# Optimization experiments

Measured on AMD Instinct MI355X. Metric: run time of the kernel, lower is better.

Reference implementation:

```python
import jax, jax.numpy as jnp
import numpy as np

OUT_F, IN_F, RANK, GROUP = 8192, 8192, 16, 128
N_GROUPS = OUT_F * IN_F // GROUP  # 524288
TOKENS = 256


def block_dequantize_2bit(weight_q2, weight_norm):
    """weight_q2: [n_groups, GROUP//4] int (uint8 values), weight_norm: [n_groups, 1] fp16.
    Each byte packs 4 two-bit codes little-endian (code k in bits 2k..2k+1).
    Code q in {0..3} dequantizes to ((q/3)*2 - 1) * norm."""
    shifts = jnp.array([0, 2, 4, 6], dtype=jnp.int32)
    q = (weight_q2[:, :, None] >> shifts) & 3          # [n_groups, GROUP//4, 4]
    q = q.reshape(weight_q2.shape[0], -1).astype(jnp.float32)  # [n_groups, GROUP]
    return (q * (2.0 / 3.0) - 1.0) * weight_norm.astype(jnp.float32)


def setup_inputs() -> dict:
    key = jax.random.key(0)
    ks = jax.random.split(key, 6)
    x = jax.random.normal(ks[0], (TOKENS, IN_F), dtype=jnp.float32)
    weight_q2 = jax.random.randint(ks[1], (N_GROUPS, GROUP // 4), 0, 256, dtype=jnp.int32)
    weight_norm = jax.random.uniform(ks[2], (N_GROUPS, 1), dtype=jnp.float16, minval=0.01, maxval=1.0)
    bias = jax.random.normal(ks[3], (OUT_F,), dtype=jnp.float32)
    lora_a = jax.random.normal(ks[4], (RANK, IN_F), dtype=jnp.float32) * 0.02
    lora_b = jax.random.normal(ks[5], (OUT_F, RANK), dtype=jnp.float32) * 0.02
    return {"x": x, "weight_q2": weight_q2, "weight_norm": weight_norm,
            "bias": bias, "lora_a": lora_a, "lora_b": lora_b}


def reference(x, weight_q2, weight_norm, bias, lora_a, lora_b):
    x_f32 = x.astype(jnp.float32)
    W = block_dequantize_2bit(weight_q2, weight_norm).reshape(OUT_F, IN_F)  # fp32 [out, in]
    base_out = x_f32 @ W.T + bias                       # [tokens, out]
    lora_out = (x_f32 @ lora_a.T) @ lora_b.T            # [tokens, out]
    return (base_out + lora_out).astype(x.dtype)
```

## Files before the change

kernel.cpp:

```cpp
#include <hip/hip_runtime.h>
#include <hip/hip_fp16.h>

typedef unsigned int u32;
typedef unsigned short u16;
typedef int i32x4 __attribute__((ext_vector_type(4)));
typedef float f32x4 __attribute__((ext_vector_type(4)));

#define OUT_F 8192
#define IN_F 8192
#define TOKENS 256
#define N_GROUPS 524288
#define SPLITK 4
#define KSPAN (IN_F / SPLITK)
#define KT (KSPAN / 64)

#define XQ_OFF 0
#define T_OFF ((size_t)TOKENS * IN_F)
#define SX_OFF (T_OFF + 32768)
#define NF_OFF (SX_OFF + 2048)
#define PART_OFF (NF_OFF + (size_t)N_GROUPS * 2)
#define PART_BYTES ((size_t)SPLITK * TOKENS * OUT_F * 4)
#define WS_NEED (PART_OFF + PART_BYTES)

__device__ __forceinline__ u32 unpack4(u32 b) {
  u32 e = ((b & 0x33u) * 0x2002u) & 0x00060006u;
  u32 o = ((b & 0xCCu) * 0x80080u) & 0x06000600u;
  return ((e | o) + 0x7D7D7D7Du) ^ 0x80808080u;
}

__global__ __launch_bounds__(256) void prep(const void* __restrict__ wn,
                                            __half* __restrict__ nf,
                                            const float* __restrict__ x,
                                            const float* __restrict__ la,
                                            signed char* __restrict__ xq,
                                            float* __restrict__ sx,
                                            float* __restrict__ t) {
  int tid = threadIdx.x;
  if (blockIdx.x < 512) {
    __shared__ int votes[3];
    __shared__ u16 tile[64][17];
    if (tid < 3) votes[tid] = 0;
    __syncthreads();
    const u16* pu = (const u16*)wn;
    const u32* pw = (const u32*)wn;
    int v16 = 0, vbf = 0, vf = 0;
    for (int i = tid; i < 2048; i += 256) {
      u16 u = pu[i];
      float h = __half2float(__builtin_bit_cast(__half, u));
      float b = __builtin_bit_cast(float, ((u32)u) << 16);
      if (h > 0.008f && h < 1.002f) v16++;
      if (b > 0.008f && b < 1.002f) vbf++;
    }
    for (int i = tid; i < 1024; i += 256) {
      float f = __builtin_bit_cast(float, pw[i]);
      if (f > 0.008f && f < 1.002f) vf++;
    }
    atomicAdd(&votes[0], v16);
    atomicAdd(&votes[1], vbf);
    atomicAdd(&votes[2], vf);
    __syncthreads();
    int a16 = votes[0], abf = votes[1], af32 = 2 * votes[2];
    int mode = (a16 >= abf && a16 >= af32) ? 0 : (abf >= af32 ? 1 : 2);
    int nb = blockIdx.x * 16;
#pragma unroll
    for (int i = 0; i < 4; ++i) {
      int idx = i * 256 + tid;
      int g = idx & 63, nl = idx >> 6;
      int flat = (nb + nl) * 64 + g;
      float v;
      if (mode == 0) v = __half2float(((const __half*)wn)[flat]);
      else if (mode == 1) v = __builtin_bit_cast(float, ((u32)((const u16*)wn)[flat]) << 16);
      else v = ((const float*)wn)[flat];
      tile[g][nl] = __builtin_bit_cast(u16, __float2half(v));
    }
    __syncthreads();
#pragma unroll
    for (int i = 0; i < 4; ++i) {
      int idx = i * 256 + tid;
      int go = idx >> 4, no = idx & 15;
      ((u16*)nf)[(size_t)go * 8192 + nb + no] = tile[go][no];
    }
    return;
  }
  int b2 = blockIdx.x - 512;
  int m = b2 & 255;
  int half = b2 >> 8;
  const float4* xr = (const float4*)(x + (size_t)m * IN_F);
  float4 xv[4];
  float am = 0.f;
  float pl[16];
#pragma unroll
  for (int r = 0; r < 16; ++r) pl[r] = 0.f;
#pragma unroll
  for (int it = 0; it < 4; ++it) {
    int k4 = half * 1024 + it * 256 + tid;
    xv[it] = xr[k4];
    am = fmaxf(am, fmaxf(fmaxf(fabsf(xv[it].x), fabsf(xv[it].y)),
                         fmaxf(fabsf(xv[it].z), fabsf(xv[it].w))));
#pragma unroll
    for (int r = 0; r < 16; ++r) {
      const float4 av = ((const float4*)(la + (size_t)r * IN_F))[k4];
      pl[r] = fmaf(xv[it].x, av.x, pl[r]);
      pl[r] = fmaf(xv[it].y, av.y, pl[r]);
      pl[r] = fmaf(xv[it].z, av.z, pl[r]);
      pl[r] = fmaf(xv[it].w, av.w, pl[r]);
    }
  }
#pragma unroll
  for (int d = 32; d > 0; d >>= 1) am = fmaxf(am, __shfl_xor(am, d));
#pragma unroll
  for (int r = 0; r < 16; ++r) {
    float v = pl[r];
#pragma unroll
    for (int d = 32; d > 0; d >>= 1) v += __shfl_xor(v, d);
    pl[r] = v;
  }
  __shared__ float red[4][16];
  __shared__ float amS[4];
  int wave = tid >> 6, lane = tid & 63;
  if (lane == 0) {
    amS[wave] = am;
#pragma unroll
    for (int r = 0; r < 16; ++r) red[wave][r] = pl[r];
  }
  __syncthreads();
  am = fmaxf(fmaxf(amS[0], amS[1]), fmaxf(amS[2], amS[3]));
  float inv = (am > 1e-20f) ? 127.f / am : 0.f;
  u32* xqw = (u32*)(xq + (size_t)m * IN_F);
#pragma unroll
  for (int it = 0; it < 4; ++it) {
    int k4 = half * 1024 + it * 256 + tid;
    int q0 = (int)rintf(xv[it].x * inv);
    int q1 = (int)rintf(xv[it].y * inv);
    int q2 = (int)rintf(xv[it].z * inv);
    int q3 = (int)rintf(xv[it].w * inv);
    xqw[k4] = (q0 & 255) | ((q1 & 255) << 8) | ((q2 & 255) << 16) | ((q3 & 255) << 24);
  }
  if (tid == 0) sx[half * 256 + m] = am / 127.f;
  if (tid < 16)
    t[((size_t)half * TOKENS + m) * 16 + tid] =
        red[0][tid] + red[1][tid] + red[2][tid] + red[3][tid];
}

__global__ __launch_bounds__(256) void prep2(const float* __restrict__ t,
                                             const float* __restrict__ lb,
                                             const float* __restrict__ bias,
                                             float* __restrict__ out) {
  __shared__ float tS[16 * 16];
  int tid = threadIdx.x;
  int n = blockIdx.x * 256 + tid;
  int mbase = blockIdx.y * 16;
  if (tid < 64) {
    float4 a = ((const float4*)(t + (size_t)mbase * 16))[tid];
    float4 b = ((const float4*)(t + (size_t)TOKENS * 16 + (size_t)mbase * 16))[tid];
    ((float4*)tS)[tid] = make_float4(a.x + b.x, a.y + b.y, a.z + b.z, a.w + b.w);
  }
  const float4* lbp = (const float4*)(lb + (size_t)n * 16);
  float4 b0 = lbp[0], b1 = lbp[1], b2 = lbp[2], b3 = lbp[3];
  float bv = bias[n];
  __syncthreads();
#pragma unroll
  for (int mm = 0; mm < 16; ++mm) {
    const float* tr = &tS[mm * 16];
    float a = bv;
    a += tr[0] * b0.x + tr[1] * b0.y + tr[2] * b0.z + tr[3] * b0.w;
    a += tr[4] * b1.x + tr[5] * b1.y + tr[6] * b1.z + tr[7] * b1.w;
    a += tr[8] * b2.x + tr[9] * b2.y + tr[10] * b2.z + tr[11] * b2.w;
    a += tr[12] * b3.x + tr[13] * b3.y + tr[14] * b3.z + tr[15] * b3.w;
    out[(size_t)(mbase + mm) * OUT_F + n] = a;
  }
}

__global__ __launch_bounds__(256) void finish(const float* __restrict__ t,
                                              const float* __restrict__ lb,
                                              const float* __restrict__ bias,
                                              const float* __restrict__ part,
                                              float* __restrict__ out) {
  __shared__ float tS[16 * 16];
  int tid = threadIdx.x;
  int n = blockIdx.x * 256 + tid;
  int mbase = blockIdx.y * 16;
  if (tid < 64) {
    float4 a = ((const float4*)(t + (size_t)mbase * 16))[tid];
    float4 b = ((const float4*)(t + (size_t)TOKENS * 16 + (size_t)mbase * 16))[tid];
    ((float4*)tS)[tid] = make_float4(a.x + b.x, a.y + b.y, a.z + b.z, a.w + b.w);
  }
  const float4* lbp = (const float4*)(lb + (size_t)n * 16);
  float4 b0 = lbp[0], b1 = lbp[1], b2 = lbp[2], b3 = lbp[3];
  float bv = bias[n];
  __syncthreads();
#pragma unroll
  for (int mm = 0; mm < 16; ++mm) {
    const float* tr = &tS[mm * 16];
    float a = bv;
    a += tr[0] * b0.x + tr[1] * b0.y + tr[2] * b0.z + tr[3] * b0.w;
    a += tr[4] * b1.x + tr[5] * b1.y + tr[6] * b1.z + tr[7] * b1.w;
    a += tr[8] * b2.x + tr[9] * b2.y + tr[10] * b2.z + tr[11] * b2.w;
    a += tr[12] * b3.x + tr[13] * b3.y + tr[14] * b3.z + tr[15] * b3.w;
    size_t base = (size_t)(mbase + mm) * OUT_F + n;
#pragma unroll
    for (int kz = 0; kz < SPLITK; ++kz)
      a += part[(size_t)kz * TOKENS * OUT_F + base];
    out[base] = a;
  }
}

__global__ __launch_bounds__(256, 2) void gemm_q2(const signed char* __restrict__ xq,
                                                  const int* __restrict__ wq,
                                                  const __half* __restrict__ nf,
                                                  const float* __restrict__ sx,
                                                  float* __restrict__ dst,
                                                  int mode) {
  __shared__ __align__(16) signed char Bs[2][128 * 64];

  int tid = threadIdx.x;
  int n0 = blockIdx.x * 128;
  int m0 = blockIdx.y * 128;
  int kz = blockIdx.z;
  int kbase = kz * KSPAN;

  int wave = tid >> 6, lane = tid & 63;
  int quad = lane >> 4, l15 = lane & 15;
  int mo = (wave & 1) * 64, no = (wave >> 1) * 64;

  const signed char* gA[4];
#pragma unroll
  for (int mt = 0; mt < 4; ++mt)
    gA[mt] = xq + (size_t)(m0 + mo + mt * 16 + l15) * IN_F + kbase + quad * 16;

  int bn = tid >> 1, h = tid & 1;
  const signed char* gB = (const signed char*)wq + (size_t)(n0 + bn) * IN_F + kbase + h * 32;
  signed char* myB0 = &Bs[0][bn * 64 + h * 32];
  signed char* myB1 = &Bs[1][bn * 64 + h * 32];

  i32x4 zi = {0, 0, 0, 0};
  f32x4 zf = {0.f, 0.f, 0.f, 0.f};
  i32x4 acc[4][4];
  f32x4 accf[4][4];
#pragma unroll
  for (int i = 0; i < 4; ++i)
#pragma unroll
    for (int j = 0; j < 4; ++j) { acc[i][j] = zi; accf[i][j] = zf; }

  i32x4 aF[4], aN[4];
#pragma unroll
  for (int mt = 0; mt < 4; ++mt) aF[mt] = *(const i32x4*)(gA[mt]);
  uint4 w0 = *(const uint4*)(gB);
  uint4 w1 = *(const uint4*)(gB + 16);
  {
    u32 c[8];
    c[0] = unpack4(w0.x); c[1] = unpack4(w0.y); c[2] = unpack4(w0.z); c[3] = unpack4(w0.w);
    c[4] = unpack4(w1.x); c[5] = unpack4(w1.y); c[6] = unpack4(w1.z); c[7] = unpack4(w1.w);
    ((uint4*)myB0)[0] = make_uint4(c[0], c[1], c[2], c[3]);
    ((uint4*)myB0)[1] = make_uint4(c[4], c[5], c[6], c[7]);
  }
  w0 = *(const uint4*)(gB + 64);
  w1 = *(const uint4*)(gB + 80);
  __syncthreads();

#pragma unroll 1
  for (int kt2 = 0; kt2 < KT / 2; ++kt2) {
    int kt = kt2 * 2;

    {
      if (kt + 1 < KT) {
#pragma unroll
        for (int mt = 0; mt < 4; ++mt)
          aN[mt] = *(const i32x4*)(gA[mt] + (kt + 1) * 64);
      }
      {
        u32 c[8];
        c[0] = unpack4(w0.x); c[1] = unpack4(w0.y); c[2] = unpack4(w0.z); c[3] = unpack4(w0.w);
        c[4] = unpack4(w1.x); c[5] = unpack4(w1.y); c[6] = unpack4(w1.z); c[7] = unpack4(w1.w);
        ((uint4*)myB1)[0] = make_uint4(c[0], c[1], c[2], c[3]);
        ((uint4*)myB1)[1] = make_uint4(c[4], c[5], c[6], c[7]);
      }
      if (kt + 2 < KT) {
        w0 = *(const uint4*)(gB + (kt + 2) * 64);
        w1 = *(const uint4*)(gB + (kt + 2) * 64 + 16);
      }
      i32x4 bf[4];
#pragma unroll
      for (int nt = 0; nt < 4; ++nt)
        bf[nt] = *(const i32x4*)(&Bs[0][(no + nt * 16 + l15) * 64 + quad * 16]);
#pragma unroll
      for (int mt = 0; mt < 4; ++mt)
#pragma unroll
        for (int nt = 0; nt < 4; ++nt)
          acc[mt][nt] = __builtin_amdgcn_mfma_i32_16x16x64_i8(aF[mt], bf[nt], acc[mt][nt], 0, 0, 0);
      __syncthreads();
    }

    {
      int ko = kt + 1;
      if (ko + 1 < KT) {
#pragma unroll
        for (int mt = 0; mt < 4; ++mt)
          aF[mt] = *(const i32x4*)(gA[mt] + (ko + 1) * 64);
      }
      int g64 = kz * (KSPAN / 128) + (ko >> 1);
      float nrm[4];
#pragma unroll
      for (int nt = 0; nt < 4; ++nt)
        nrm[nt] = __half2float(nf[(size_t)g64 * 8192 + n0 + no + nt * 16 + l15]) * (1.f / 3.f);
      if (ko + 1 < KT) {
        u32 c[8];
        c[0] = unpack4(w0.x); c[1] = unpack4(w0.y); c[2] = unpack4(w0.z); c[3] = unpack4(w0.w);
        c[4] = unpack4(w1.x); c[5] = unpack4(w1.y); c[6] = unpack4(w1.z); c[7] = unpack4(w1.w);
        ((uint4*)myB0)[0] = make_uint4(c[0], c[1], c[2], c[3]);
        ((uint4*)myB0)[1] = make_uint4(c[4], c[5], c[6], c[7]);
      }
      if (ko + 2 < KT) {
        w0 = *(const uint4*)(gB + (ko + 2) * 64);
        w1 = *(const uint4*)(gB + (ko + 2) * 64 + 16);
      }
      i32x4 bf[4];
#pragma unroll
      for (int nt = 0; nt < 4; ++nt)
        bf[nt] = *(const i32x4*)(&Bs[1][(no + nt * 16 + l15) * 64 + quad * 16]);
#pragma unroll
      for (int mt = 0; mt < 4; ++mt)
#pragma unroll
        for (int nt = 0; nt < 4; ++nt)
          acc[mt][nt] = __builtin_amdgcn_mfma_i32_16x16x64_i8(aN[mt], bf[nt], acc[mt][nt], 0, 0, 0);
#pragma unroll
      for (int nt = 0; nt < 4; ++nt)
#pragma unroll
        for (int mt = 0; mt < 4; ++mt) {
#pragma unroll
          for (int r = 0; r < 4; ++r)
            accf[mt][nt][r] = fmaf((float)acc[mt][nt][r], nrm[nt], accf[mt][nt][r]);
          acc[mt][nt] = zi;
        }
      __syncthreads();
    }
  }

  const float* sxh = sx + (kz >> 1) * 256;
  if (mode) {
    float* pp = dst + (size_t)kz * TOKENS * OUT_F;
#pragma unroll
    for (int mt = 0; mt < 4; ++mt)
#pragma unroll
      for (int r = 0; r < 4; ++r) {
        int mm = m0 + mo + mt * 16 + quad * 4 + r;
        float s = sxh[mm];
#pragma unroll
        for (int nt = 0; nt < 4; ++nt) {
          int nn = n0 + no + nt * 16 + l15;
          pp[(size_t)mm * OUT_F + nn] = accf[mt][nt][r] * s;
        }
      }
  } else {
#pragma unroll
    for (int mt = 0; mt < 4; ++mt)
#pragma unroll
      for (int r = 0; r < 4; ++r) {
        int mm = m0 + mo + mt * 16 + quad * 4 + r;
        float s = sxh[mm];
#pragma unroll
        for (int nt = 0; nt < 4; ++nt) {
          int nn = n0 + no + nt * 16 + l15;
          atomicAdd(&dst[(size_t)mm * OUT_F + nn], accf[mt][nt][r] * s);
        }
      }
  }
}

extern "C" void kernel_launch(void* const* d_in, const int* in_sizes, int n_in,
                              void* d_out, int out_size, void* d_ws, size_t ws_size,
                              hipStream_t stream) {
  (void)in_sizes; (void)n_in; (void)out_size;
  const float* x = (const float*)d_in[0];
  const int* wq = (const int*)d_in[1];
  const void* wn_raw = d_in[2];
  const float* bias = (const float*)d_in[3];
  const float* la = (const float*)d_in[4];
  const float* lb = (const float*)d_in[5];
  float* out = (float*)d_out;

  signed char* xq = (signed char*)((char*)d_ws + XQ_OFF);
  float* t = (float*)((char*)d_ws + T_OFF);
  float* sx = (float*)((char*)d_ws + SX_OFF);
  __half* nf = (__half*)((char*)d_ws + NF_OFF);
  float* part = (float*)((char*)d_ws + PART_OFF);
  int usep = ws_size >= WS_NEED;

  prep<<<1024, 256, 0, stream>>>(wn_raw, nf, x, la, xq, sx, t);
  if (usep) {
    gemm_q2<<<dim3(OUT_F / 128, TOKENS / 128, SPLITK), 256, 0, stream>>>(xq, wq, nf, sx, part, 1);
    finish<<<dim3(OUT_F / 256, TOKENS / 16), 256, 0, stream>>>(t, lb, bias, part, out);
  } else {
    prep2<<<dim3(OUT_F / 256, TOKENS / 16), 256, 0, stream>>>(t, lb, bias, out);
    gemm_q2<<<dim3(OUT_F / 128, TOKENS / 128, SPLITK), 256, 0, stream>>>(xq, wq, nf, sx, out, 0);
  }
}
```

Measured before the change: 172.9 us.

## Load 2-bit weights directly into MFMA registers and split LoRA-A into atomic blocks

The GEMM kernel no longer stages unpacked weights through shared memory with barriers. Each wave loads its own B fragments straight from global memory into registers, unpacks them there, and prefetches the next k-step along with the group norms. Separately, the x·lora_aᵀ product moves out of the quantization blocks into 64 extra blocks that reduce over k-chunks with atomicAdd into a zeroed buffer. This removes LDS traffic and syncthreads from the main loop, at the cost of redundant weight loads across the waves that share an n-tile, an extra memset launch, and nondeterministic float summation order.

New measurement: 216.5 us. 1.25x slower.

```diff
diff --git a/kernel.cpp b/kernel.cpp
--- a/kernel.cpp
+++ b/kernel.cpp
@@ -16,7 +16,7 @@
 
 #define XQ_OFF 0
 #define T_OFF ((size_t)TOKENS * IN_F)
-#define SX_OFF (T_OFF + 32768)
+#define SX_OFF (T_OFF + 16384)
 #define NF_OFF (SX_OFF + 2048)
 #define PART_OFF (NF_OFF + (size_t)N_GROUPS * 2)
 #define PART_BYTES ((size_t)SPLITK * TOKENS * OUT_F * 4)
@@ -82,64 +82,57 @@
     }
     return;
   }
-  int b2 = blockIdx.x - 512;
-  int m = b2 & 255;
-  int half = b2 >> 8;
-  const float4* xr = (const float4*)(x + (size_t)m * IN_F);
-  float4 xv[4];
-  float am = 0.f;
-  float pl[16];
-#pragma unroll
-  for (int r = 0; r < 16; ++r) pl[r] = 0.f;
-#pragma unroll
-  for (int it = 0; it < 4; ++it) {
-    int k4 = half * 1024 + it * 256 + tid;
-    xv[it] = xr[k4];
-    am = fmaxf(am, fmaxf(fmaxf(fabsf(xv[it].x), fabsf(xv[it].y)),
-                         fmaxf(fabsf(xv[it].z), fabsf(xv[it].w))));
+  if (blockIdx.x < 1024) {
+    int b2 = blockIdx.x - 512;
+    int m = b2 & 255;
+    int half = b2 >> 8;
+    const float4* xr = (const float4*)(x + (size_t)m * IN_F);
+    float4 xv[4];
+    float am = 0.f;
+#pragma unroll
+    for (int it = 0; it < 4; ++it) {
+      xv[it] = xr[half * 1024 + it * 256 + tid];
+      am = fmaxf(am, fmaxf(fmaxf(fabsf(xv[it].x), fabsf(xv[it].y)),
+                           fmaxf(fabsf(xv[it].z), fabsf(xv[it].w))));
+    }
+#pragma unroll
+    for (int d = 32; d > 0; d >>= 1) am = fmaxf(am, __shfl_xor(am, d));
+    __shared__ float amS[4];
+    int wave = tid >> 6;
+    if ((tid & 63) == 0) amS[wave] = am;
+    __syncthreads();
+    am = fmaxf(fmaxf(amS[0], amS[1]), fmaxf(amS[2], amS[3]));
+    float inv = (am > 1e-20f) ? 127.f / am : 0.f;
+    u32* xqw = (u32*)(xq + (size_t)m * IN_F);
+#pragma unroll
+    for (int it = 0; it < 4; ++it) {
+      int k4 = half * 1024 + it * 256 + tid;
+      int q0 = (int)rintf(xv[it].x * inv);
+      int q1 = (int)rintf(xv[it].y * inv);
+      int q2 = (int)rintf(xv[it].z * inv);
+      int q3 = (int)rintf(xv[it].w * inv);
+      xqw[k4] = (q0 & 255) | ((q1 & 255) << 8) | ((q2 & 255) << 16) | ((q3 & 255) << 24);
+    }
+    if (tid == 0) sx[half * 256 + m] = am / 127.f;
+    return;
+  }
+  int c = blockIdx.x - 1024;
+  int k0 = c * 128;
+  int m = tid;
+  const float4* xr = (const float4*)(x + (size_t)m * IN_F + k0);
+  float s[16];
+#pragma unroll
+  for (int r = 0; r < 16; ++r) s[r] = 0.f;
+  for (int jj = 0; jj < 32; ++jj) {
+    float4 xv = xr[jj];
 #pragma unroll
     for (int r = 0; r < 16; ++r) {
-      const float4 av = ((const float4*)(la + (size_t)r * IN_F))[k4];
-      pl[r] = fmaf(xv[it].x, av.x, pl[r]);
-      pl[r] = fmaf(xv[it].y, av.y, pl[r]);
-      pl[r] = fmaf(xv[it].z, av.z, pl[r]);
-      pl[r] = fmaf(xv[it].w, av.w, pl[r]);
-    }
-  }
-#pragma unroll
-  for (int d = 32; d > 0; d >>= 1) am = fmaxf(am, __shfl_xor(am, d));
-#pragma unroll
-  for (int r = 0; r < 16; ++r) {
-    float v = pl[r];
-#pragma unroll
-    for (int d = 32; d > 0; d >>= 1) v += __shfl_xor(v, d);
-    pl[r] = v;
-  }
-  __shared__ float red[4][16];
-  __shared__ float amS[4];
-  int wave = tid >> 6, lane = tid & 63;
-  if (lane == 0) {
-    amS[wave] = am;
-#pragma unroll
-    for (int r = 0; r < 16; ++r) red[wave][r] = pl[r];
-  }
-  __syncthreads();
-  am = fmaxf(fmaxf(amS[0], amS[1]), fmaxf(amS[2], amS[3]));
-  float inv = (am > 1e-20f) ? 127.f / am : 0.f;
-  u32* xqw = (u32*)(xq + (size_t)m * IN_F);
-#pragma unroll
-  for (int it = 0; it < 4; ++it) {
-    int k4 = half * 1024 + it * 256 + tid;
-    int q0 = (int)rintf(xv[it].x * inv);
-    int q1 = (int)rintf(xv[it].y * inv);
-    int q2 = (int)rintf(xv[it].z * inv);
-    int q3 = (int)rintf(xv[it].w * inv);
-    xqw[k4] = (q0 & 255) | ((q1 & 255) << 8) | ((q2 & 255) << 16) | ((q3 & 255) << 24);
-  }
-  if (tid == 0) sx[half * 256 + m] = am / 127.f;
-  if (tid < 16)
-    t[((size_t)half * TOKENS + m) * 16 + tid] =
-        red[0][tid] + red[1][tid] + red[2][tid] + red[3][tid];
+      float4 lv = *(const float4*)(la + (size_t)r * IN_F + k0 + jj * 4);
+      s[r] += xv.x * lv.x + xv.y * lv.y + xv.z * lv.z + xv.w * lv.w;
+    }
+  }
+#pragma unroll
+  for (int r = 0; r < 16; ++r) atomicAdd(&t[(size_t)m * 16 + r], s[r]);
 }
 
 __global__ __launch_bounds__(256) void prep2(const float* __restrict__ t,
@@ -150,11 +143,7 @@
   int tid = threadIdx.x;
   int n = blockIdx.x * 256 + tid;
   int mbase = blockIdx.y * 16;
-  if (tid < 64) {
-    float4 a = ((const float4*)(t + (size_t)mbase * 16))[tid];
-    float4 b = ((const float4*)(t + (size_t)TOKENS * 16 + (size_t)mbase * 16))[tid];
-    ((float4*)tS)[tid] = make_float4(a.x + b.x, a.y + b.y, a.z + b.z, a.w + b.w);
-  }
+  if (tid < 64) ((float4*)tS)[tid] = ((const float4*)(t + (size_t)mbase * 16))[tid];
   const float4* lbp = (const float4*)(lb + (size_t)n * 16);
   float4 b0 = lbp[0], b1 = lbp[1], b2 = lbp[2], b3 = lbp[3];
   float bv = bias[n];
@@ -180,11 +169,7 @@
   int tid = threadIdx.x;
   int n = blockIdx.x * 256 + tid;
   int mbase = blockIdx.y * 16;
-  if (tid < 64) {
-    float4 a = ((const float4*)(t + (size_t)mbase * 16))[tid];
-    float4 b = ((const float4*)(t + (size_t)TOKENS * 16 + (size_t)mbase * 16))[tid];
-    ((float4*)tS)[tid] = make_float4(a.x + b.x, a.y + b.y, a.z + b.z, a.w + b.w);
-  }
+  if (tid < 64) ((float4*)tS)[tid] = ((const float4*)(t + (size_t)mbase * 16))[tid];
   const float4* lbp = (const float4*)(lb + (size_t)n * 16);
   float4 b0 = lbp[0], b1 = lbp[1], b2 = lbp[2], b3 = lbp[3];
   float bv = bias[n];
@@ -211,8 +196,6 @@
                                                   const float* __restrict__ sx,
                                                   float* __restrict__ dst,
                                                   int mode) {
-  __shared__ __align__(16) signed char Bs[2][128 * 64];
-
   int tid = threadIdx.x;
   int n0 = blockIdx.x * 128;
   int m0 = blockIdx.y * 128;
@@ -224,14 +207,13 @@
   int mo = (wave & 1) * 64, no = (wave >> 1) * 64;
 
   const signed char* gA[4];
-#pragma unroll
-  for (int mt = 0; mt < 4; ++mt)
-    gA[mt] = xq + (size_t)(m0 + mo + mt * 16 + l15) * IN_F + kbase + quad * 16;
-
-  int bn = tid >> 1, h = tid & 1;
-  const signed char* gB = (const signed char*)wq + (size_t)(n0 + bn) * IN_F + kbase + h * 32;
-  signed char* myB0 = &Bs[0][bn * 64 + h * 32];
-  signed char* myB1 = &Bs[1][bn * 64 + h * 32];
+  const signed char* gB[4];
+#pragma unroll
+  for (int i = 0; i < 4; ++i) {
+    gA[i] = xq + (size_t)(m0 + mo + i * 16 + l15) * IN_F + kbase + quad * 16;
+    gB[i] = (const signed char*)wq + (size_t)(n0 + no + i * 16 + l15) * IN_F + kbase + quad * 16;
+  }
+  const __half* nfg = nf + (size_t)(kz * (KSPAN / 128)) * 8192 + n0 + no + l15;
 
   i32x4 zi = {0, 0, 0, 0};
   f32x4 zf = {0.f, 0.f, 0.f, 0.f};
@@ -242,97 +224,78 @@
 #pragma unroll
     for (int j = 0; j < 4; ++j) { acc[i][j] = zi; accf[i][j] = zf; }
 
-  i32x4 aF[4], aN[4];
-#pragma unroll
-  for (int mt = 0; mt < 4; ++mt) aF[mt] = *(const i32x4*)(gA[mt]);
-  uint4 w0 = *(const uint4*)(gB);
-  uint4 w1 = *(const uint4*)(gB + 16);
-  {
-    u32 c[8];
-    c[0] = unpack4(w0.x); c[1] = unpack4(w0.y); c[2] = unpack4(w0.z); c[3] = unpack4(w0.w);
-    c[4] = unpack4(w1.x); c[5] = unpack4(w1.y); c[6] = unpack4(w1.z); c[7] = unpack4(w1.w);
-    ((uint4*)myB0)[0] = make_uint4(c[0], c[1], c[2], c[3]);
-    ((uint4*)myB0)[1] = make_uint4(c[4], c[5], c[6], c[7]);
-  }
-  w0 = *(const uint4*)(gB + 64);
-  w1 = *(const uint4*)(gB + 80);
-  __syncthreads();
+  uint4 wE[4], wO[4];
+#pragma unroll
+  for (int i = 0; i < 4; ++i) {
+    wE[i] = *(const uint4*)(gB[i]);
+    wO[i] = *(const uint4*)(gB[i] + 64);
+  }
+  float nC[4], nN[4];
+#pragma unroll
+  for (int i = 0; i < 4; ++i) nC[i] = __half2float(nfg[i * 16]) * (1.f / 3.f);
 
 #pragma unroll 1
   for (int kt2 = 0; kt2 < KT / 2; ++kt2) {
     int kt = kt2 * 2;
+    int koE = (kt + 2 < KT ? kt + 2 : KT - 2) * 64;
+    int koO = (kt + 3 < KT ? kt + 3 : KT - 1) * 64;
+    int g2 = (kt2 + 1 < KT / 2 ? kt2 + 1 : kt2);
 
     {
-      if (kt + 1 < KT) {
-#pragma unroll
-        for (int mt = 0; mt < 4; ++mt)
-          aN[mt] = *(const i32x4*)(gA[mt] + (kt + 1) * 64);
-      }
-      {
-        u32 c[8];
-        c[0] = unpack4(w0.x); c[1] = unpack4(w0.y); c[2] = unpack4(w0.z); c[3] = unpack4(w0.w);
-        c[4] = unpack4(w1.x); c[5] = unpack4(w1.y); c[6] = unpack4(w1.z); c[7] = unpack4(w1.w);
-        ((uint4*)myB1)[0] = make_uint4(c[0], c[1], c[2], c[3]);
-        ((uint4*)myB1)[1] = make_uint4(c[4], c[5], c[6], c[7]);
-      }
-      if (kt + 2 < KT) {
-        w0 = *(const uint4*)(gB + (kt + 2) * 64);
-        w1 = *(const uint4*)(gB + (kt + 2) * 64 + 16);
-      }
+      uint4 tW0 = *(const uint4*)(gB[0] + koE);
+      uint4 tW1 = *(const uint4*)(gB[1] + koE);
+      uint4 tW2 = *(const uint4*)(gB[2] + koE);
+      uint4 tW3 = *(const uint4*)(gB[3] + koE);
+      i32x4 aC[4];
+#pragma unroll
+      for (int i = 0; i < 4; ++i) aC[i] = *(const i32x4*)(gA[i] + kt * 64);
+#pragma unroll
+      for (int i = 0; i < 4; ++i)
+        nN[i] = __half2float(nfg[(size_t)g2 * 8192 + i * 16]) * (1.f / 3.f);
       i32x4 bf[4];
 #pragma unroll
-      for (int nt = 0; nt < 4; ++nt)
-        bf[nt] = *(const i32x4*)(&Bs[0][(no + nt * 16 + l15) * 64 + quad * 16]);
+      for (int i = 0; i < 4; ++i)
+        bf[i] = (i32x4){(int)unpack4(wE[i].x), (int)unpack4(wE[i].y),
+                        (int)unpack4(wE[i].z), (int)unpack4(wE[i].w)};
 #pragma unroll
       for (int mt = 0; mt < 4; ++mt)
 #pragma unroll
         for (int nt = 0; nt < 4; ++nt)
-          acc[mt][nt] = __builtin_amdgcn_mfma_i32_16x16x64_i8(aF[mt], bf[nt], acc[mt][nt], 0, 0, 0);
-      __syncthreads();
+          acc[mt][nt] = __builtin_amdgcn_mfma_i32_16x16x64_i8(aC[mt], bf[nt], acc[mt][nt], 0, 0, 0);
+      wE[0] = tW0; wE[1] = tW1; wE[2] = tW2; wE[3] = tW3;
     }
 
     {
-      int ko = kt + 1;
-      if (ko + 1 < KT) {
-#pragma unroll
-        for (int mt = 0; mt < 4; ++mt)
-          aF[mt] = *(const i32x4*)(gA[mt] + (ko + 1) * 64);
-      }
-      int g64 = kz * (KSPAN / 128) + (ko >> 1);
-      float nrm[4];
-#pragma unroll
-      for (int nt = 0; nt < 4; ++nt)
-        nrm[nt] = __half2float(nf[(size_t)g64 * 8192 + n0 + no + nt * 16 + l15]) * (1.f / 3.f);
-      if (ko + 1 < KT) {
-        u32 c[8];
-        c[0] = unpack4(w0.x); c[1] = unpack4(w0.y); c[2] = unpack4(w0.z); c[3] = unpack4(w0.w);
-        c[4] = unpack4(w1.x); c[5] = unpack4(w1.y); c[6] = unpack4(w1.z); c[7] = unpack4(w1.w);
-        ((uint4*)myB0)[0] = make_uint4(c[0], c[1], c[2], c[3]);
-        ((uint4*)myB0)[1] = make_uint4(c[4], c[5], c[6], c[7]);
-      }
-      if (ko + 2 < KT) {
-        w0 = *(const uint4*)(gB + (ko + 2) * 64);
-        w1 = *(const uint4*)(gB + (ko + 2) * 64 + 16);
-      }
+      uint4 tW0 = *(const uint4*)(gB[0] + koO);
+      uint4 tW1 = *(const uint4*)(gB[1] + koO);
+      uint4 tW2 = *(const uint4*)(gB[2] + koO);
+      uint4 tW3 = *(const uint4*)(gB[3] + koO);
+      i32x4 aC[4];
+#pragma unroll
+      for (int i = 0; i < 4; ++i) aC[i] = *(const i32x4*)(gA[i] + (kt + 1) * 64);
       i32x4 bf[4];
 #pragma unroll
-      for (int nt = 0; nt < 4; ++nt)
-        bf[nt] = *(const i32x4*)(&Bs[1][(no + nt * 16 + l15) * 64 + quad * 16]);
+      for (int i = 0; i < 4; ++i)
+        bf[i] = (i32x4){(int)unpack4(wO[i].x), (int)unpack4(wO[i].y),
+                        (int)unpack4(wO[i].z), (int)unpack4(wO[i].w)};
 #pragma unroll
       for (int mt = 0; mt < 4; ++mt)
 #pragma unroll
         for (int nt = 0; nt < 4; ++nt)
-          acc[mt][nt] = __builtin_amdgcn_mfma_i32_16x16x64_i8(aN[mt], bf[nt], acc[mt][nt], 0, 0, 0);
-#pragma unroll
-      for (int nt = 0; nt < 4; ++nt)
+          acc[mt][nt] = __builtin_amdgcn_mfma_i32_16x16x64_i8(aC[mt], bf[nt], acc[mt][nt], 0, 0, 0);
+      wO[0] = tW0; wO[1] = tW1; wO[2] = tW2; wO[3] = tW3;
+#pragma unroll
+      for (int nt = 0; nt < 4; ++nt) {
+        float s = nC[nt];
 #pragma unroll
         for (int mt = 0; mt < 4; ++mt) {
 #pragma unroll
           for (int r = 0; r < 4; ++r)
-            accf[mt][nt][r] = fmaf((float)acc[mt][nt][r], nrm[nt], accf[mt][nt][r]);
+            accf[mt][nt][r] = fmaf((float)acc[mt][nt][r], s, accf[mt][nt][r]);
           acc[mt][nt] = zi;
         }
-      __syncthreads();
+        nC[nt] = nN[nt];
+      }
     }
   }
 
@@ -386,7 +349,8 @@
   float* part = (float*)((char*)d_ws + PART_OFF);
   int usep = ws_size >= WS_NEED;
 
-  prep<<<1024, 256, 0, stream>>>(wn_raw, nf, x, la, xq, sx, t);
+  hipMemsetAsync(t, 0, (size_t)TOKENS * 16 * 4, stream);
+  prep<<<1088, 256, 0, stream>>>(wn_raw, nf, x, la, xq, sx, t);
   if (usep) {
     gemm_q2<<<dim3(OUT_F / 128, TOKENS / 128, SPLITK), 256, 0, stream>>>(xq, wq, nf, sx, part, 1);
     finish<<<dim3(OUT_F / 256, TOKENS / 16), 256, 0, stream>>>(t, lb, bias, part, out);
```
